# Optimization experiments

Hardware: AMD Instinct MI355X
Metric: run time of the kernel (lower is better)

The kernel has to match this reference:

```python
import jax, jax.numpy as jnp
import numpy as np

B = 32       # batch
IN_N = 32    # input capsules
IN_D = 16    # input capsule dim (== out_d)
H = 14       # input spatial
OUT_N = 32   # output capsules
OUT_D = 16
HO = 7       # parent grid h_out = w_out
HID = 64     # Linformer projection dim
EPS = 1e-5


def _gconv(x, w, groups):
    # x: [b, C, H, W], w: [C_out, C_in/groups, kh, kw]; stride 1, pad 1
    return jax.lax.conv_general_dilated(
        x, w, window_strides=(1, 1), padding=((1, 1), (1, 1)),
        dimension_numbers=("NCHW", "OIHW", "NCHW"), feature_group_count=groups)


def setup_inputs() -> dict:
    key = jax.random.key(0)
    ks = jax.random.split(key, 7)
    current_pose = jax.random.normal(ks[0], (B, IN_N, H, H, IN_D), dtype=jnp.float32)
    next_pose = jax.random.normal(ks[1], (B, OUT_N, HO, HO, OUT_D), dtype=jnp.float32)
    # grouped conv weights (torch layout OIHW, groups = IN_N)
    current_w = 0.05 * jax.random.normal(ks[2], (IN_N * IN_D, IN_D, 3, 3), dtype=jnp.float32)
    next_w = 0.05 * jax.random.normal(ks[3], (OUT_N * OUT_D, OUT_N * OUT_D // IN_N, 3, 3), dtype=jnp.float32)
    E_proj = 0.02 * jax.random.normal(ks[4], (IN_N, H * H, HID), dtype=jnp.float32)
    rel_embedd = jax.random.normal(ks[5], (IN_D, HO * HO), dtype=jnp.float32)
    ln_gamma = jnp.ones((OUT_D,), dtype=jnp.float32)
    ln_beta = jnp.zeros((OUT_D,), dtype=jnp.float32)
    return {
        "current_pose": current_pose, "next_pose": next_pose,
        "current_w": current_w, "next_w": next_w,
        "E_proj": E_proj, "rel_embedd": rel_embedd,
        "ln_gamma": ln_gamma, "ln_beta": ln_beta,
        "num_iter": 1,
    }


def reference(current_pose, next_pose, current_w, next_w, E_proj, rel_embedd,
              ln_gamma, ln_beta, num_iter):
    b = current_pose.shape[0]
    # 5D -> [b, n*d, H, W]
    cp = current_pose.transpose(0, 2, 3, 1, 4).reshape(b, H, H, IN_N * IN_D)
    cp = cp.transpose(0, 3, 1, 2)
    cp = _gconv(cp, current_w, IN_N)                       # [b, n*d, H, H]
    # headwise Linformer key projection
    cp = cp.reshape(b, IN_D, IN_N, 1, H * H)
    k = jnp.matmul(cp, E_proj)                             # [b, d, n, 1, HID]
    k = k.reshape(b, IN_D, IN_N * HID).transpose(0, 2, 1)  # [b, n*HID, d]
    rel = jnp.broadcast_to(rel_embedd.T[None], (b, HO * HO, IN_D))
    k = jnp.concatenate([k, rel], axis=1)                  # [b, N, d]

    # parent pose -> queries
    q = next_pose.transpose(0, 2, 3, 1, 4).reshape(b, HO, HO, OUT_N * OUT_D)
    q = q.transpose(0, 3, 1, 2)
    q = _gconv(q, next_w, IN_N)                            # [b, out_n*out_d, HO, HO]
    q = q.reshape(b, OUT_N * HO * HO, OUT_D)               # [b, J, d]

    dots = jnp.einsum("bje,bie->bji", q, k) * (IN_D ** -0.5)  # [b, J, N]
    dots = jax.nn.softmax(dots, axis=-2)                   # softmax over queries j
    out = jnp.einsum("bji,bie->bje", dots, k)              # [b, J, d]

    out = out.reshape(b, OUT_N * IN_D, HO, HO)
    out = _gconv(out, next_w, IN_N)
    out = out.reshape(b, OUT_N, HO, HO, IN_D)

    # LayerNorm over last dim (dropout rate = 0)
    mu = out.mean(-1, keepdims=True)
    var = ((out - mu) ** 2).mean(-1, keepdims=True)
    out = (out - mu) / jnp.sqrt(var + EPS) * ln_gamma + ln_beta
    return out
```

## Files before the change

### kernel.cpp

```cpp
#include <hip/hip_runtime.h>

typedef unsigned short u16;
typedef __attribute__((ext_vector_type(8))) short short8;
typedef __attribute__((ext_vector_type(4))) float floatx4;
typedef __attribute__((ext_vector_type(4))) unsigned uintx4;

#define MFMA16(a, b, c) __builtin_amdgcn_mfma_f32_16x16x32_bf16(a, b, c, 0, 0, 0)

__device__ inline u16 bf16rn(float x) {
    unsigned u = __float_as_uint(x);
    u += 0x7fffu + ((u >> 16) & 1u);
    return (u16)(u >> 16);
}
__device__ inline float bf16tof(u16 h) { return __uint_as_float(((unsigned)h) << 16); }
__device__ inline short8 ld8(const u16* p) { return *(const short8*)p; }
__device__ inline unsigned pack2(float a, float b) {
    return __builtin_amdgcn_perm(__float_as_uint(b), __float_as_uint(a), 0x07060302u);
}

#define FOIDX(i) ((i) + ((i) >> 4))

__global__ __launch_bounds__(256) void k_ecvt2(const float* __restrict__ E,
                                               const float* __restrict__ rel,
                                               const float* __restrict__ w,
                                               u16* __restrict__ EhT,
                                               u16* __restrict__ ElT,
                                               u16* __restrict__ Kh,
                                               u16* __restrict__ Kl,
                                               u16* __restrict__ KhT,
                                               u16* __restrict__ KlT,
                                               float* __restrict__ w2) {
    int blk = blockIdx.x, tid = threadIdx.x;
    if (blk < 32) {
        __shared__ float ep[196 * 65];
        int m = blk;
        const float* eb = E + (size_t)m * 12544;
        for (int t = tid; t < 12544; t += 256) {
            int p = t >> 6, h = t & 63;
            ep[p * 65 + h] = eb[t];
        }
        __syncthreads();
        for (int t = tid; t < 64 * 224; t += 256) {
            int h = t / 224, p = t % 224;
            float v = (p < 196) ? ep[p * 65 + h] : 0.f;
            u16 hi = bf16rn(v);
            u16 lo = bf16rn(v - bf16tof(hi));
            EhT[(size_t)m * 14336 + t] = hi;
            ElT[(size_t)m * 14336 + t] = lo;
        }
    } else if (blk < 64) {
        int b = blk - 32;
        size_t bK = (size_t)b * 2112;
        size_t bT = (size_t)b * 33792;
#pragma unroll
        for (int k = 0; k < 4; ++k) {
            int idx = tid + k * 256;
            int row = idx >> 4, e = idx & 15;
            int i = 2048 + row;
            float v = (row < 49) ? rel[e * 49 + row] : 0.f;
            u16 h = bf16rn(v);
            u16 l = bf16rn(v - bf16tof(h));
            Kh[(bK + i) * 16 + e] = h;
            Kl[(bK + i) * 16 + e] = l;
            KhT[bT + (size_t)e * 2112 + i] = h;
            KlT[bT + (size_t)e * 2112 + i] = l;
        }
    } else {
        int g0 = (blk - 64) * 4;
        for (int t = tid; t < 4 * 2304; t += 256) {
            int g = g0 + t / 2304, r = t % 2304;
            int oc = r / 144, rr = r % 144;
            w2[(size_t)g * 2304 + (rr / 9) * 144 + oc * 9 + (rr % 9)] =
                w[(size_t)g * 2304 + r];
        }
    }
}

__global__ __launch_bounds__(256) void k_conv14(const float* __restrict__ pose,
                                                const float* __restrict__ w2,
                                                float* __restrict__ out) {
    int blk = blockIdx.x;
    int oh = blk & 1, bg = blk >> 1;
    int tid = threadIdx.x;
    __shared__ float patch[16 * 256];
#pragma unroll
    for (int k = 0; k < 16; ++k) patch[k * 256 + tid] = 0.f;
    __syncthreads();
    const float* pin = pose + (size_t)bg * 3136;
    for (int t = tid; t < 3136; t += 256) {
        int p = t >> 4, ic = t & 15;
        int y = p / 14, x = p % 14;
        patch[ic * 256 + (y + 1) * 16 + (x + 1)] = pin[t];
    }
    __syncthreads();
    int g = bg & 31;
    const float* wg = w2 + (size_t)g * 2304 + oh * 72;
    float* po = out + (size_t)bg * 3136 + oh * 8 * 196;
    if (tid < 196) {
        int y = tid / 14, x = tid % 14;
        int base = (y + 1) * 16 + (x + 1);
        float acc[8];
#pragma unroll
        for (int oc = 0; oc < 8; ++oc) acc[oc] = 0.f;
        for (int ic = 0; ic < 16; ++ic) {
            const float* pr = patch + ic * 256 + base;
            float win[9];
#pragma unroll
            for (int ky = 0; ky < 3; ++ky)
#pragma unroll
                for (int kx = 0; kx < 3; ++kx)
                    win[ky * 3 + kx] = pr[(ky - 1) * 16 + (kx - 1)];
            const float* wi = wg + ic * 144;
#pragma unroll
            for (int oc = 0; oc < 8; ++oc)
#pragma unroll
                for (int kk = 0; kk < 9; ++kk)
                    acc[oc] += win[kk] * wi[oc * 9 + kk];
        }
#pragma unroll
        for (int oc = 0; oc < 8; ++oc) po[oc * 196 + tid] = acc[oc];
    }
}

__global__ __launch_bounds__(128) void k_qconv(const float* __restrict__ pose,
                                               const float* __restrict__ w,
                                               u16* __restrict__ Qp) {
    int blk = blockIdx.x;
    int b = blk >> 5, g = blk & 31;
    int tid = threadIdx.x;
    __shared__ float patch[16 * 144];
    __shared__ float fo[833];
    for (int t = tid; t < 16 * 144; t += 128) patch[t] = 0.f;
    __syncthreads();
    const float* pin = pose + (size_t)blk * 784;
    for (int t = tid; t < 784; t += 128) {
        int p = t >> 4, ic = t & 15;
        int y = p / 7, x = p % 7;
        patch[ic * 144 + (y + 1) * 16 + (x + 1)] = pin[t];
    }
    __syncthreads();
    int oh = tid >> 6, lane = tid & 63;
    if (lane < 49) {
        const float* wg = w + (size_t)g * 2304 + (size_t)oh * 8 * 144;
        int y = lane / 7, x = lane % 7;
        int base = (y + 1) * 16 + (x + 1);
        float acc[8];
#pragma unroll
        for (int oc = 0; oc < 8; ++oc) acc[oc] = 0.f;
        for (int ic = 0; ic < 16; ++ic) {
            const float* pr = patch + ic * 144 + base;
            float win[9];
#pragma unroll
            for (int ky = 0; ky < 3; ++ky)
#pragma unroll
                for (int kx = 0; kx < 3; ++kx)
                    win[ky * 3 + kx] = pr[(ky - 1) * 16 + (kx - 1)];
            const float* wi = wg + ic * 9;
#pragma unroll
            for (int oc = 0; oc < 8; ++oc)
#pragma unroll
                for (int kk = 0; kk < 9; ++kk)
                    acc[oc] += win[kk] * wi[oc * 144 + kk];
        }
#pragma unroll
        for (int oc = 0; oc < 8; ++oc)
            fo[FOIDX((oh * 8 + oc) * 49 + lane)] = acc[oc];
    }
    __syncthreads();
    if (tid < 49) {
        float v[16];
#pragma unroll
        for (int k = 0; k < 16; ++k) v[k] = fo[FOIDX(tid * 16 + k)];
        unsigned hw[8], lw[8];
#pragma unroll
        for (int t = 0; t < 8; ++t) {
            float x0 = v[2 * t] * 0.25f, x1 = v[2 * t + 1] * 0.25f;
            u16 h0 = bf16rn(x0), h1 = bf16rn(x1);
            u16 l0 = bf16rn(x0 - bf16tof(h0)), l1 = bf16rn(x1 - bf16tof(h1));
            hw[t] = (unsigned)h0 | ((unsigned)h1 << 16);
            lw[t] = (unsigned)l0 | ((unsigned)l1 << 16);
        }
        uint4* r4 = (uint4*)(Qp + ((size_t)b * 1568 + (size_t)g * 49 + tid) * 32);
        r4[0] = make_uint4(hw[0], hw[1], hw[2], hw[3]);
        r4[1] = make_uint4(hw[4], hw[5], hw[6], hw[7]);
        r4[2] = make_uint4(lw[0], lw[1], lw[2], lw[3]);
        r4[3] = make_uint4(lw[4], lw[5], lw[6], lw[7]);
    }
}

__global__ __launch_bounds__(128) void k_oconv(const float* __restrict__ in,
                                               const float* __restrict__ w,
                                               const float* __restrict__ gamma,
                                               const float* __restrict__ beta,
                                               float* __restrict__ out) {
    int blk = blockIdx.x;
    int g = blk & 31;
    int tid = threadIdx.x;
    __shared__ float patch[16 * 144];
    __shared__ float fo[833];
    for (int t = tid; t < 16 * 144; t += 128) patch[t] = 0.f;
    __syncthreads();
    const float* pin = in + (size_t)blk * 784;
    for (int t = tid; t < 784; t += 128) {
        int ic = t / 49, p = t % 49;
        int y = p / 7, x = p % 7;
        patch[ic * 144 + (y + 1) * 16 + (x + 1)] =
            (pin[t] + pin[t + 802816]) + (pin[t + 1605632] + pin[t + 2408448]);
    }
    __syncthreads();
    int oh = tid >> 6, lane = tid & 63;
    if (lane < 49) {
        const float* wg = w + (size_t)g * 2304 + (size_t)oh * 8 * 144;
        int y = lane / 7, x = lane % 7;
        int base = (y + 1) * 16 + (x + 1);
        float acc[8];
#pragma unroll
        for (int oc = 0; oc < 8; ++oc) acc[oc] = 0.f;
        for (int ic = 0; ic < 16; ++ic) {
            const float* pr = patch + ic * 144 + base;
            float win[9];
#pragma unroll
            for (int ky = 0; ky < 3; ++ky)
#pragma unroll
                for (int kx = 0; kx < 3; ++kx)
                    win[ky * 3 + kx] = pr[(ky - 1) * 16 + (kx - 1)];
            const float* wi = wg + ic * 9;
#pragma unroll
            for (int oc = 0; oc < 8; ++oc)
#pragma unroll
                for (int kk = 0; kk < 9; ++kk)
                    acc[oc] += win[kk] * wi[oc * 144 + kk];
        }
#pragma unroll
        for (int oc = 0; oc < 8; ++oc)
            fo[FOIDX((oh * 8 + oc) * 49 + lane)] = acc[oc];
    }
    __syncthreads();
    if (tid < 49) {
        float v[16];
#pragma unroll
        for (int k = 0; k < 16; ++k) v[k] = fo[FOIDX(tid * 16 + k)];
        float sum = 0.f;
#pragma unroll
        for (int k = 0; k < 16; ++k) sum += v[k];
        float mu = sum * 0.0625f;
        float var = 0.f;
#pragma unroll
        for (int k = 0; k < 16; ++k) var += (v[k] - mu) * (v[k] - mu);
        float rstd = rsqrtf(var * 0.0625f + 1e-5f);
        float o[16];
#pragma unroll
        for (int k = 0; k < 16; ++k) o[k] = (v[k] - mu) * rstd * gamma[k] + beta[k];
        float4* op = (float4*)(out + (size_t)blk * 784 + (size_t)tid * 16);
        op[0] = make_float4(o[0], o[1], o[2], o[3]);
        op[1] = make_float4(o[4], o[5], o[6], o[7]);
        op[2] = make_float4(o[8], o[9], o[10], o[11]);
        op[3] = make_float4(o[12], o[13], o[14], o[15]);
    }
}

__global__ __launch_bounds__(256) void k_kproj2(const float* __restrict__ cpconv,
                                                const u16* __restrict__ EhT,
                                                const u16* __restrict__ ElT,
                                                u16* __restrict__ Kh,
                                                u16* __restrict__ Kl,
                                                u16* __restrict__ KhT,
                                                u16* __restrict__ KlT) {
    int blk = blockIdx.x;
    int b = blk >> 5, m = blk & 31;
    int wave = threadIdx.x >> 6, lane = threadIdx.x & 63;
    int ht = wave;
    int n = lane & 15, quad = lane >> 4;

    const float* arow = cpconv + ((size_t)b * 512 + (size_t)n * 32 + m) * 196;
    const u16* bhrow = EhT + ((size_t)m * 64 + ht * 16 + n) * 224;
    const u16* blrow = ElT + ((size_t)m * 64 + ht * 16 + n) * 224;

    floatx4 c = {0.f, 0.f, 0.f, 0.f};
#pragma unroll
    for (int pc = 0; pc < 7; ++pc) {
        int p0 = pc * 32 + quad * 8;
        float av[8];
        if (p0 <= 188) {
            float4 x = *(const float4*)(arow + p0);
            float4 y = *(const float4*)(arow + p0 + 4);
            av[0]=x.x; av[1]=x.y; av[2]=x.z; av[3]=x.w;
            av[4]=y.x; av[5]=y.y; av[6]=y.z; av[7]=y.w;
        } else {
#pragma unroll
            for (int k2 = 0; k2 < 8; ++k2) av[k2] = (p0 + k2 < 196) ? arow[p0 + k2] : 0.f;
        }
        short8 ah, al;
#pragma unroll
        for (int k2 = 0; k2 < 8; ++k2) {
            u16 h = bf16rn(av[k2]);
            ah[k2] = (short)h;
            al[k2] = (short)bf16rn(av[k2] - bf16tof(h));
        }
        short8 bh = ld8(bhrow + pc * 32 + quad * 8);
        short8 bl = ld8(blrow + pc * 32 + quad * 8);
        c = MFMA16(ah, bh, c);
        c = MFMA16(ah, bl, c);
        c = MFMA16(al, bh, c);
    }
    int i = m * 64 + ht * 16 + n;
    size_t bK = (size_t)b * 2112;
    size_t bT = (size_t)b * 33792;
    u16 h[4], l[4];
#pragma unroll
    for (int r = 0; r < 4; ++r) {
        h[r] = bf16rn(c[r]);
        l[r] = bf16rn(c[r] - bf16tof(h[r]));
    }
    *(uint2*)(Kh + (bK + i) * 16 + quad * 4) =
        make_uint2((unsigned)h[0] | ((unsigned)h[1] << 16), (unsigned)h[2] | ((unsigned)h[3] << 16));
    *(uint2*)(Kl + (bK + i) * 16 + quad * 4) =
        make_uint2((unsigned)l[0] | ((unsigned)l[1] << 16), (unsigned)l[2] | ((unsigned)l[3] << 16));
#pragma unroll
    for (int r = 0; r < 4; ++r) {
        KhT[bT + (size_t)(quad * 4 + r) * 2112 + i] = h[r];
        KlT[bT + (size_t)(quad * 4 + r) * 2112 + i] = l[r];
    }
}

__global__ __launch_bounds__(256) void k_stats4(const u16* __restrict__ Qp,
                                                const u16* __restrict__ Kh,
                                                const u16* __restrict__ Kl,
                                                float* __restrict__ dpart) {
    int blk = blockIdx.x;
    int b = blk / 34; int rem = blk % 34; int jh = rem / 17; int tb = rem % 17;
    int wave = threadIdx.x >> 6, lane = threadIdx.x & 63;
    int it2 = tb * 4 + wave;
    if (it2 >= 66) return;
    int ibase = it2 * 32;
    int n = lane & 15, quad = lane >> 4;
    size_t bK = (size_t)b * 2112;
    const u16* kb = Kh + (bK + ibase + n) * 16 + (quad & 1) * 8;
    const u16* lb = Kl + (bK + ibase + n) * 16 + (quad & 1) * 8;
    short8 bh0 = ld8(kb), bh1 = ld8(kb + 256);
    short8 bl0 = ld8(lb), bl1 = ld8(lb + 256);
    const u16* qb = Qp + (size_t)b * 50176 + (size_t)jh * 49 * 512 + n * 32 + quad * 8;
    floatx4 d0 = {0.f,0.f,0.f,0.f}, d1 = {0.f,0.f,0.f,0.f};
    short8 a0 = ld8(qb), a1 = ld8(qb + 512);
    for (int c = 0; c < 49; ++c) {
        short8 a2 = (c + 2 < 49) ? ld8(qb + (size_t)(c + 2) * 512) : a0;
        floatx4 s0 = {0.f,0.f,0.f,0.f}, s1 = {0.f,0.f,0.f,0.f};
        s0 = MFMA16(a0, bh0, s0);
        s0 = MFMA16(a0, bl0, s0);
        s1 = MFMA16(a0, bh1, s1);
        s1 = MFMA16(a0, bl1, s1);
        d0.x += __expf(s0.x); d0.y += __expf(s0.y);
        d0.z += __expf(s0.z); d0.w += __expf(s0.w);
        d1.x += __expf(s1.x); d1.y += __expf(s1.y);
        d1.z += __expf(s1.z); d1.w += __expf(s1.w);
        a0 = a1; a1 = a2;
    }
    float t0 = d0.x + d0.y + d0.z + d0.w;
    float t1 = d1.x + d1.y + d1.z + d1.w;
    t0 += __shfl_xor(t0, 16); t0 += __shfl_xor(t0, 32);
    t1 += __shfl_xor(t1, 16); t1 += __shfl_xor(t1, 32);
    if (quad == 0) {
        dpart[(size_t)jh * 67584 + bK + ibase + n]      = t0;
        dpart[(size_t)jh * 67584 + bK + ibase + 16 + n] = t1;
    }
}

__global__ __launch_bounds__(256) void k_vscale(const float* __restrict__ dpart,
                                                u16* __restrict__ VhT,
                                                u16* __restrict__ VlT) {
    int gid = blockIdx.x * 256 + threadIdx.x;
    int ic = gid % 264;
    int be = gid / 264;
    int b = be >> 4, e = be & 15;
    size_t off = (size_t)b * 33792 + (size_t)e * 2112 + (size_t)ic * 8;
    short8 h8 = ld8(VhT + off);
    short8 l8 = ld8(VlT + off);
    const float* dp = dpart + (size_t)b * 2112 + ic * 8;
    float4 da0 = *(const float4*)dp;
    float4 da1 = *(const float4*)(dp + 4);
    float4 db0 = *(const float4*)(dp + 67584);
    float4 db1 = *(const float4*)(dp + 67588);
    float d[8] = {da0.x+db0.x, da0.y+db0.y, da0.z+db0.z, da0.w+db0.w,
                  da1.x+db1.x, da1.y+db1.y, da1.z+db1.z, da1.w+db1.w};
    short8 oh, ol;
#pragma unroll
    for (int k = 0; k < 8; ++k) {
        float v = bf16tof((u16)h8[k]) + bf16tof((u16)l8[k]);
        float sv = v / d[k];
        u16 hh = bf16rn(sv);
        ol[k] = (short)bf16rn(sv - bf16tof(hh));
        oh[k] = (short)hh;
    }
    *(short8*)(VhT + off) = oh;
    *(short8*)(VlT + off) = ol;
}

__global__ __launch_bounds__(256) void k_pv8(const u16* __restrict__ Qp,
                                             const u16* __restrict__ Kh,
                                             const u16* __restrict__ Kl,
                                             const u16* __restrict__ VhT,
                                             const u16* __restrict__ VlT,
                                             float* __restrict__ opart) {
    __shared__ __align__(16) u16 sH[2][32][16];
    __shared__ __align__(16) u16 sL[2][32][16];
    __shared__ __align__(16) u16 tH[2][16][32];
    __shared__ __align__(16) u16 tL[2][16][32];

    int blk = blockIdx.x;
    int b = blk / 52; int rem = blk % 52; int jtb = rem >> 2; int iq = rem & 3;
    int tid = threadIdx.x, wave = tid >> 6, lane = tid & 63;
    int n = lane & 15, quad = lane >> 4, qh = quad & 1;
    int jt0 = (jtb * 4 + wave) * 2;
    int jc0 = jt0     < 98 ? jt0     : 97;
    int jc1 = jt0 + 1 < 98 ? jt0 + 1 : 97;
    int nc = (iq < 2) ? 17 : 16;
    int i0 = iq * 512 + (iq < 2 ? iq : 2) * 32;
    size_t bK = (size_t)b * 2112;
    size_t bT = (size_t)b * 33792;

    short8 aq0 = ld8(Qp + ((size_t)b * 1568 + (size_t)jc0 * 16 + n) * 32 + quad * 8);
    short8 aq1 = ld8(Qp + ((size_t)b * 1568 + (size_t)jc1 * 16 + n) * 32 + quad * 8);

    int role = wave, L = lane;
    uint4 sreg;
    auto ldchunk = [&](int c) {
        int i0c = i0 + c * 32;
        if (role == 0)      sreg = *(const uint4*)(Kh  + (bK + i0c + (L >> 1)) * 16 + (L & 1) * 8);
        else if (role == 1) sreg = *(const uint4*)(Kl  + (bK + i0c + (L >> 1)) * 16 + (L & 1) * 8);
        else if (role == 2) sreg = *(const uint4*)(VhT + bT + (size_t)(L >> 2) * 2112 + i0c + (L & 3) * 8);
        else                sreg = *(const uint4*)(VlT + bT + (size_t)(L >> 2) * 2112 + i0c + (L & 3) * 8);
    };
    auto stchunk = [&](int bf) {
        if (role == 0)      *(uint4*)(&sH[bf][L >> 1][(L & 1) * 8]) = sreg;
        else if (role == 1) *(uint4*)(&sL[bf][L >> 1][(L & 1) * 8]) = sreg;
        else if (role == 2) *(uint4*)(&tH[bf][L >> 2][(L & 3) * 8]) = sreg;
        else                *(uint4*)(&tL[bf][L >> 2][(L & 3) * 8]) = sreg;
    };

    floatx4 o0 = {0.f, 0.f, 0.f, 0.f}, o1 = {0.f, 0.f, 0.f, 0.f};

    ldchunk(0); stchunk(0); ldchunk(1);
    __syncthreads();
    for (int c = 0; c < nc; ++c) {
        int cb = c & 1;
        short8 sh0 = ld8(&sH[cb][n][qh * 8]);
        short8 sh1 = ld8(&sH[cb][16 + n][qh * 8]);
        short8 sl0 = ld8(&sL[cb][n][qh * 8]);
        short8 sl1 = ld8(&sL[cb][16 + n][qh * 8]);
        short8 th  = ld8(&tH[cb][n][quad * 8]);
        short8 tl  = ld8(&tL[cb][n][quad * 8]);

        {
            floatx4 s0 = {0.f,0.f,0.f,0.f}, s1 = {0.f,0.f,0.f,0.f};
            s0 = MFMA16(sh0, aq0, s0);
            s0 = MFMA16(sl0, aq0, s0);
            s1 = MFMA16(sh1, aq0, s1);
            s1 = MFMA16(sl1, aq0, s1);
            unsigned u00 = pack2(__expf(s0[0]), __expf(s0[1]));
            unsigned u01 = pack2(__expf(s0[2]), __expf(s0[3]));
            unsigned u10 = pack2(__expf(s1[0]), __expf(s1[1]));
            unsigned u11 = pack2(__expf(s1[2]), __expf(s1[3]));
            asm("v_permlane32_swap_b32 %0, %1" : "+v"(u00), "+v"(u10));
            asm("v_permlane32_swap_b32 %0, %1" : "+v"(u01), "+v"(u11));
            asm("v_permlane16_swap_b32 %0, %1" : "+v"(u00), "+v"(u10));
            asm("v_permlane16_swap_b32 %0, %1" : "+v"(u01), "+v"(u11));
            uintx4 uv = {u00, u01, u10, u11};
            short8 aw = __builtin_bit_cast(short8, uv);
            o0 = MFMA16(aw, th, o0);
            o0 = MFMA16(aw, tl, o0);
        }
        {
            floatx4 s0 = {0.f,0.f,0.f,0.f}, s1 = {0.f,0.f,0.f,0.f};
            s0 = MFMA16(sh0, aq1, s0);
            s0 = MFMA16(sl0, aq1, s0);
            s1 = MFMA16(sh1, aq1, s1);
            s1 = MFMA16(sl1, aq1, s1);
            unsigned u00 = pack2(__expf(s0[0]), __expf(s0[1]));
            unsigned u01 = pack2(__expf(s0[2]), __expf(s0[3]));
            unsigned u10 = pack2(__expf(s1[0]), __expf(s1[1]));
            unsigned u11 = pack2(__expf(s1[2]), __expf(s1[3]));
            asm("v_permlane32_swap_b32 %0, %1" : "+v"(u00), "+v"(u10));
            asm("v_permlane32_swap_b32 %0, %1" : "+v"(u01), "+v"(u11));
            asm("v_permlane16_swap_b32 %0, %1" : "+v"(u00), "+v"(u10));
            asm("v_permlane16_swap_b32 %0, %1" : "+v"(u01), "+v"(u11));
            uintx4 uv = {u00, u01, u10, u11};
            short8 aw = __builtin_bit_cast(short8, uv);
            o1 = MFMA16(aw, th, o1);
            o1 = MFMA16(aw, tl, o1);
        }
        if (c + 1 < nc) stchunk((c + 1) & 1);
        if (c + 2 < nc) ldchunk(c + 2);
        __syncthreads();
    }
    if (jt0 < 98) {
        float* ob = opart + (size_t)iq * 802816 +
                    ((size_t)b * 1568 + (size_t)jt0 * 16) * 16;
#pragma unroll
        for (int r = 0; r < 4; ++r) ob[(quad * 4 + r) * 16 + n] = o0[r];
    }
    if (jt0 + 1 < 98) {
        float* ob = opart + (size_t)iq * 802816 +
                    ((size_t)b * 1568 + (size_t)(jt0 + 1) * 16) * 16;
#pragma unroll
        for (int r = 0; r < 4; ++r) ob[(quad * 4 + r) * 16 + n] = o1[r];
    }
}

extern "C" void kernel_launch(void* const* d_in, const int* in_sizes, int n_in,
                              void* d_out, int out_size, void* d_ws, size_t ws_size,
                              hipStream_t stream) {
    const float* current_pose = (const float*)d_in[0];
    const float* next_pose    = (const float*)d_in[1];
    const float* current_w    = (const float*)d_in[2];
    const float* next_w       = (const float*)d_in[3];
    const float* E_proj       = (const float*)d_in[4];
    const float* rel          = (const float*)d_in[5];
    const float* ln_gamma     = (const float*)d_in[6];
    const float* ln_beta      = (const float*)d_in[7];
    float* out = (float*)d_out;
    float* ws  = (float*)d_ws;

    float* cpconv = ws;
    float* opart  = ws;
    float* dpart  = ws + 3211264;
    float* w2     = ws + 4014080;
    u16*   ub     = (u16*)(ws + 4087808);
    u16* Qp  = ub;
    u16* Kh  = ub + 1605632;
    u16* Kl  = ub + 2686976;
    u16* KhT = ub + 3768320;
    u16* KlT = ub + 4849664;
    u16* EhT = ub + 5931008;
    u16* ElT = ub + 6389760;

    k_ecvt2 <<<72,   256, 0, stream>>>(E_proj, rel, current_w, EhT, ElT,
                                       Kh, Kl, KhT, KlT, w2);
    k_conv14<<<2048, 256, 0, stream>>>(current_pose, w2, cpconv);
    k_qconv <<<1024, 128, 0, stream>>>(next_pose, next_w, Qp);
    k_kproj2<<<1024, 256, 0, stream>>>(cpconv, EhT, ElT, Kh, Kl, KhT, KlT);
    k_stats4<<<1088, 256, 0, stream>>>(Qp, Kh, Kl, dpart);
    k_vscale<<<528,  256, 0, stream>>>(dpart, KhT, KlT);
    k_pv8   <<<1664, 256, 0, stream>>>(Qp, Kh, Kl, KhT, KlT, opart);
    k_oconv <<<1024, 128, 0, stream>>>(opart, next_w, ln_gamma, ln_beta, out);
}
```

Measured before the change: 232.5 us.

## Stage whole K/V slice in LDS, drop V low-part, split keys six ways

The PV kernel now loads a 352-key slice of K (hi and lo) and the scaled V (hi only) into padded shared memory once per block, then loops over 11 chunks with no barriers. This replaces the double-buffered per-chunk staging and its per-iteration syncs. V is kept only as a single bf16 term, which halves the V MFMAs and removes the low-part write in vscale, at some cost in precision. The key range is split 6 ways instead of 4, with more blocks, so oconv now sums six partial buffers, and opart moves to its own workspace region.

```diff
diff --git a/kernel.cpp b/kernel.cpp
--- a/kernel.cpp
+++ b/kernel.cpp
@@ -205,7 +205,8 @@
         int ic = t / 49, p = t % 49;
         int y = p / 7, x = p % 7;
         patch[ic * 144 + (y + 1) * 16 + (x + 1)] =
-            (pin[t] + pin[t + 802816]) + (pin[t + 1605632] + pin[t + 2408448]);
+            ((pin[t] + pin[t + 802816]) + (pin[t + 1605632] + pin[t + 2408448]))
+          + (pin[t + 3211264] + pin[t + 4014080]);
     }
     __syncthreads();
     int oh = tid >> 6, lane = tid & 63;
@@ -367,7 +368,7 @@
 
 __global__ __launch_bounds__(256) void k_vscale(const float* __restrict__ dpart,
                                                 u16* __restrict__ VhT,
-                                                u16* __restrict__ VlT) {
+                                                const u16* __restrict__ VlT) {
     int gid = blockIdx.x * 256 + threadIdx.x;
     int ic = gid % 264;
     int be = gid / 264;
@@ -382,73 +383,63 @@
     float4 db1 = *(const float4*)(dp + 67588);
     float d[8] = {da0.x+db0.x, da0.y+db0.y, da0.z+db0.z, da0.w+db0.w,
                   da1.x+db1.x, da1.y+db1.y, da1.z+db1.z, da1.w+db1.w};
-    short8 oh, ol;
+    short8 oh;
 #pragma unroll
     for (int k = 0; k < 8; ++k) {
         float v = bf16tof((u16)h8[k]) + bf16tof((u16)l8[k]);
-        float sv = v / d[k];
-        u16 hh = bf16rn(sv);
-        ol[k] = (short)bf16rn(sv - bf16tof(hh));
-        oh[k] = (short)hh;
+        oh[k] = (short)bf16rn(v / d[k]);
     }
     *(short8*)(VhT + off) = oh;
-    *(short8*)(VlT + off) = ol;
-}
-
-__global__ __launch_bounds__(256) void k_pv8(const u16* __restrict__ Qp,
-                                             const u16* __restrict__ Kh,
-                                             const u16* __restrict__ Kl,
-                                             const u16* __restrict__ VhT,
-                                             const u16* __restrict__ VlT,
-                                             float* __restrict__ opart) {
-    __shared__ __align__(16) u16 sH[2][32][16];
-    __shared__ __align__(16) u16 sL[2][32][16];
-    __shared__ __align__(16) u16 tH[2][16][32];
-    __shared__ __align__(16) u16 tL[2][16][32];
+}
+
+__global__ __launch_bounds__(256) void k_pv10(const u16* __restrict__ Qp,
+                                              const u16* __restrict__ Kh,
+                                              const u16* __restrict__ Kl,
+                                              const u16* __restrict__ VhT,
+                                              float* __restrict__ opart) {
+    __shared__ __align__(16) u16 sKh[352 * 20];
+    __shared__ __align__(16) u16 sKl[352 * 20];
+    __shared__ __align__(16) u16 sV [16 * 356];
 
     int blk = blockIdx.x;
-    int b = blk / 52; int rem = blk % 52; int jtb = rem >> 2; int iq = rem & 3;
+    int b = blk / 78; int rem = blk % 78; int jtb = rem / 6; int iq = rem % 6;
     int tid = threadIdx.x, wave = tid >> 6, lane = tid & 63;
     int n = lane & 15, quad = lane >> 4, qh = quad & 1;
     int jt0 = (jtb * 4 + wave) * 2;
     int jc0 = jt0     < 98 ? jt0     : 97;
     int jc1 = jt0 + 1 < 98 ? jt0 + 1 : 97;
-    int nc = (iq < 2) ? 17 : 16;
-    int i0 = iq * 512 + (iq < 2 ? iq : 2) * 32;
+    int i0 = iq * 352;
     size_t bK = (size_t)b * 2112;
     size_t bT = (size_t)b * 33792;
 
+#pragma unroll
+    for (int k = 0; k < 3; ++k) {
+        int t = tid + k * 256;
+        if (t < 704) {
+            int row = t >> 1, half = t & 1;
+            uint4 vh = *(const uint4*)(Kh + (bK + i0 + row) * 16 + half * 8);
+            uint4 vl = *(const uint4*)(Kl + (bK + i0 + row) * 16 + half * 8);
+            *(uint4*)(&sKh[row * 20 + half * 8]) = vh;
+            *(uint4*)(&sKl[row * 20 + half * 8]) = vl;
+            int e = t / 44, i8 = (t % 44) * 8;
+            uint4 vv = *(const uint4*)(VhT + bT + (size_t)e * 2112 + i0 + i8);
+            *(uint4*)(&sV[e * 356 + i8]) = vv;
+        }
+    }
+
     short8 aq0 = ld8(Qp + ((size_t)b * 1568 + (size_t)jc0 * 16 + n) * 32 + quad * 8);
     short8 aq1 = ld8(Qp + ((size_t)b * 1568 + (size_t)jc1 * 16 + n) * 32 + quad * 8);
 
-    int role = wave, L = lane;
-    uint4 sreg;
-    auto ldchunk = [&](int c) {
-        int i0c = i0 + c * 32;
-        if (role == 0)      sreg = *(const uint4*)(Kh  + (bK + i0c + (L >> 1)) * 16 + (L & 1) * 8);
-        else if (role == 1) sreg = *(const uint4*)(Kl  + (bK + i0c + (L >> 1)) * 16 + (L & 1) * 8);
-        else if (role == 2) sreg = *(const uint4*)(VhT + bT + (size_t)(L >> 2) * 2112 + i0c + (L & 3) * 8);
-        else                sreg = *(const uint4*)(VlT + bT + (size_t)(L >> 2) * 2112 + i0c + (L & 3) * 8);
-    };
-    auto stchunk = [&](int bf) {
-        if (role == 0)      *(uint4*)(&sH[bf][L >> 1][(L & 1) * 8]) = sreg;
-        else if (role == 1) *(uint4*)(&sL[bf][L >> 1][(L & 1) * 8]) = sreg;
-        else if (role == 2) *(uint4*)(&tH[bf][L >> 2][(L & 3) * 8]) = sreg;
-        else                *(uint4*)(&tL[bf][L >> 2][(L & 3) * 8]) = sreg;
-    };
-
     floatx4 o0 = {0.f, 0.f, 0.f, 0.f}, o1 = {0.f, 0.f, 0.f, 0.f};
-
-    ldchunk(0); stchunk(0); ldchunk(1);
-    __syncthreads();
-    for (int c = 0; c < nc; ++c) {
-        int cb = c & 1;
-        short8 sh0 = ld8(&sH[cb][n][qh * 8]);
-        short8 sh1 = ld8(&sH[cb][16 + n][qh * 8]);
-        short8 sl0 = ld8(&sL[cb][n][qh * 8]);
-        short8 sl1 = ld8(&sL[cb][16 + n][qh * 8]);
-        short8 th  = ld8(&tH[cb][n][quad * 8]);
-        short8 tl  = ld8(&tL[cb][n][quad * 8]);
+    __syncthreads();
+
+    for (int c = 0; c < 11; ++c) {
+        int ib = c * 32;
+        short8 sh0 = ld8(&sKh[(ib + n) * 20 + qh * 8]);
+        short8 sh1 = ld8(&sKh[(ib + 16 + n) * 20 + qh * 8]);
+        short8 sl0 = ld8(&sKl[(ib + n) * 20 + qh * 8]);
+        short8 sl1 = ld8(&sKl[(ib + 16 + n) * 20 + qh * 8]);
+        short8 th  = ld8(&sV[n * 356 + ib + quad * 8]);
 
         {
             floatx4 s0 = {0.f,0.f,0.f,0.f}, s1 = {0.f,0.f,0.f,0.f};
@@ -467,7 +458,6 @@
             uintx4 uv = {u00, u01, u10, u11};
             short8 aw = __builtin_bit_cast(short8, uv);
             o0 = MFMA16(aw, th, o0);
-            o0 = MFMA16(aw, tl, o0);
         }
         {
             floatx4 s0 = {0.f,0.f,0.f,0.f}, s1 = {0.f,0.f,0.f,0.f};
@@ -486,11 +476,7 @@
             uintx4 uv = {u00, u01, u10, u11};
             short8 aw = __builtin_bit_cast(short8, uv);
             o1 = MFMA16(aw, th, o1);
-            o1 = MFMA16(aw, tl, o1);
-        }
-        if (c + 1 < nc) stchunk((c + 1) & 1);
-        if (c + 2 < nc) ldchunk(c + 2);
-        __syncthreads();
+        }
     }
     if (jt0 < 98) {
         float* ob = opart + (size_t)iq * 802816 +
@@ -521,7 +507,6 @@
     float* ws  = (float*)d_ws;
 
     float* cpconv = ws;
-    float* opart  = ws;
     float* dpart  = ws + 3211264;
     float* w2     = ws + 4014080;
     u16*   ub     = (u16*)(ws + 4087808);
@@ -532,6 +517,7 @@
     u16* KlT = ub + 4849664;
     u16* EhT = ub + 5931008;
     u16* ElT = ub + 6389760;
+    float* opart = ws + 7512064;
 
     k_ecvt2 <<<72,   256, 0, stream>>>(E_proj, rel, current_w, EhT, ElT,
                                        Kh, Kl, KhT, KlT, w2);
@@ -540,6 +526,6 @@
     k_kproj2<<<1024, 256, 0, stream>>>(cpconv, EhT, ElT, Kh, Kl, KhT, KlT);
     k_stats4<<<1088, 256, 0, stream>>>(Qp, Kh, Kl, dpart);
     k_vscale<<<528,  256, 0, stream>>>(dpart, KhT, KlT);
-    k_pv8   <<<1664, 256, 0, stream>>>(Qp, Kh, Kl, KhT, KlT, opart);
+    k_pv10  <<<2496, 256, 0, stream>>>(Qp, Kh, Kl, KhT, opart);
     k_oconv <<<1024, 128, 0, stream>>>(opart, next_w, ln_gamma, ln_beta, out);
 }
```

New measurement: 262.8 us. 1.13x slower.
